# Kernel tuning notes

Hardware: AMD Instinct MI355X
Metric: run time of the kernel (lower is better)

Reference implementation:

```python
import math
import jax, jax.numpy as jnp
import numpy as np

INPUT_DIM = 1024
OUTPUT_DIM = 1024
DEGREE = 8
EPS = 1.0


def setup_inputs() -> dict:
    key = jax.random.key(0)
    k1, k2 = jax.random.split(key)
    x = jax.random.normal(k1, (8192, INPUT_DIM), dtype=jnp.float32)
    std = 1.0 / (INPUT_DIM * (DEGREE + 1))
    hermite_coeffs = std * jax.random.normal(k2, (INPUT_DIM, OUTPUT_DIM, DEGREE + 1), dtype=jnp.float32)
    return {"x": x, "hermite_coeffs": hermite_coeffs}


def _hermite_basis(x):
    # x: [B, I] squashed input; returns [B, I, DEGREE+1] Hermite-function basis.
    pi_q = math.pi ** (-0.25)
    gauss = jnp.exp(-0.5 * x * x)
    h0 = pi_q * gauss
    hs = [h0]
    if DEGREE > 0:
        hs.append(math.sqrt(2.0) * pi_q * x * gauss)
    for i in range(2, DEGREE + 1):
        hs.append(math.sqrt(2.0 / i) * x * hs[i - 1] - math.sqrt((i - 1) / i) * hs[i - 2])
    return jnp.stack(hs, axis=-1)


def reference(x, hermite_coeffs):
    x = x.reshape(-1, INPUT_DIM)
    x = jnp.tanh(x) * (math.sqrt(2 * DEGREE + 1) + EPS)
    hermite = _hermite_basis(x)  # [B, I, D+1]
    y = jnp.einsum('bid,iod->bo', hermite, hermite_coeffs)
    return y.reshape(-1, OUTPUT_DIM)
```

## Files before the change

### kernel.cpp

```cpp
#include <hip/hip_runtime.h>

#define MDIM 8192
#define IDIM 1024
#define ODIM 1024
#define D1   9
#define KDIM (IDIM * D1)

typedef _Float16 half8 __attribute__((ext_vector_type(8)));
typedef float    float4v __attribute__((ext_vector_type(4)));

#define BSCALE 256.0f
#define INV_BSCALE (1.0f / 256.0f)

__device__ __forceinline__ void hermite9(float xv, float h[D1]) {
    float ax = fabsf(xv);
    float t  = __expf(-2.0f * ax);
    float th = (1.0f - t) / (1.0f + t);
    th = copysignf(th, xv);
    float u = th * 5.123105625617661f;
    float g = __expf(-0.5f * u * u);
    h[0] = 0.7511255444649425f * g;
    h[1] = 1.0622519497598084f * u * g;
    const float c1[D1] = {0.f, 0.f, 1.0f, 0.8164965809277260f, 0.7071067811865476f,
                          0.6324555320336759f, 0.5773502691896258f, 0.5345224838248488f, 0.5f};
    const float c2[D1] = {0.f, 0.f, 0.7071067811865476f, 0.8164965809277260f, 0.8660254037844386f,
                          0.8944271909999159f, 0.9128709291752769f, 0.9258200997725514f, 0.9354143466934853f};
#pragma unroll
    for (int d = 2; d < D1; ++d) h[d] = c1[d] * u * h[d - 1] - c2[d] * h[d - 2];
}

__global__ void prep_b(const float* __restrict__ C, _Float16* __restrict__ Bt) {
    int t = blockIdx.x * 256 + threadIdx.x;
    int o = t >> 10;
    int i = t & 1023;
    const float* cp = C + ((size_t)i * ODIM + o) * D1;
    _Float16* bp = Bt + (size_t)o * KDIM + i;
#pragma unroll
    for (int d = 0; d < D1; ++d)
        bp[(size_t)d * IDIM] = (_Float16)(cp[d] * BSCALE);
}

__global__ void prep_h(const float* __restrict__ x, _Float16* __restrict__ H,
                       int row0, int nrows) {
    int t = blockIdx.x * 256 + threadIdx.x;
    int r = t >> 7;
    int ig = (t & 127) << 3;
    if (r >= nrows) return;
    const float* xp = x + ((size_t)(row0 + r) << 10) + ig;
    float4 a0 = *(const float4*)xp;
    float4 a1 = *(const float4*)(xp + 4);
    float xv[8] = {a0.x, a0.y, a0.z, a0.w, a1.x, a1.y, a1.z, a1.w};
    float h[8][D1];
#pragma unroll
    for (int e = 0; e < 8; ++e) hermite9(xv[e], h[e]);
    _Float16* hp = H + (size_t)r * KDIM + ig;
#pragma unroll
    for (int d = 0; d < D1; ++d) {
        half8 v;
#pragma unroll
        for (int e = 0; e < 8; ++e) v[e] = (_Float16)h[e][d];
        *(half8*)(hp + (size_t)d * IDIM) = v;
    }
}

__global__ __launch_bounds__(256, 2) void gemm_hf(
    const _Float16* __restrict__ A,
    const _Float16* __restrict__ Bt,
    float* __restrict__ out)
{
    const int tid = threadIdx.x;
    const int w = tid >> 6;
    const int l = tid & 63;
    const int bn = blockIdx.x;
    const int bm = blockIdx.y;

    __shared__ _Float16 As[128 * 64];
    __shared__ _Float16 Bs[128 * 64];

    const int lrow8 = l >> 3;
    const int kgrp  = (l & 7) ^ lrow8;
    const _Float16* Ag = A  + ((size_t)(bm * 128 + w * 8 + lrow8) * KDIM + kgrp * 8);
    const _Float16* Bg = Bt + ((size_t)(bn * 128 + w * 8 + lrow8) * KDIM + kgrp * 8);

    const int q   = l >> 4;
    const int m16 = l & 15;
    const int s3  = m16 & 7;
    const int wm  = w >> 1, wn = w & 1;

    float4v acc[4][4] = {};

    for (int k0 = 0; k0 < KDIM; k0 += 64) {
#pragma unroll
        for (int r = 0; r < 4; ++r) {
            __builtin_amdgcn_global_load_lds(
                (const __attribute__((address_space(1))) void*)(Ag + (size_t)(r * 32) * KDIM + k0),
                (__attribute__((address_space(3))) void*)((char*)As + (r * 4 + w) * 1024),
                16, 0, 0);
            __builtin_amdgcn_global_load_lds(
                (const __attribute__((address_space(1))) void*)(Bg + (size_t)(r * 32) * KDIM + k0),
                (__attribute__((address_space(3))) void*)((char*)Bs + (r * 4 + w) * 1024),
                16, 0, 0);
        }
        __syncthreads();

#pragma unroll
        for (int ko = 0; ko < 2; ++ko) {
            const int slot = (q + 4 * ko) ^ s3;
            half8 af[4], bf[4];
#pragma unroll
            for (int i = 0; i < 4; ++i) {
                af[i] = *(const half8*)&As[(wm * 64 + i * 16 + m16) * 64 + slot * 8];
                bf[i] = *(const half8*)&Bs[(wn * 64 + i * 16 + m16) * 64 + slot * 8];
            }
#pragma unroll
            for (int i = 0; i < 4; ++i)
#pragma unroll
                for (int j = 0; j < 4; ++j)
                    acc[i][j] = __builtin_amdgcn_mfma_f32_16x16x32_f16(af[i], bf[j], acc[i][j], 0, 0, 0);
        }
        __syncthreads();
    }

#pragma unroll
    for (int i = 0; i < 4; ++i) {
        int row = bm * 128 + wm * 64 + i * 16 + q * 4;
#pragma unroll
        for (int j = 0; j < 4; ++j) {
            int col = bn * 128 + wn * 64 + j * 16 + m16;
            float* op = out + (size_t)row * ODIM + col;
#pragma unroll
            for (int r2 = 0; r2 < 4; ++r2)
                op[(size_t)r2 * ODIM] = acc[i][j][r2] * INV_BSCALE;
        }
    }
}

__global__ void naive_kernel(const float* __restrict__ x, const float* __restrict__ C,
                             float* __restrict__ out) {
    __shared__ float hb[IDIM * D1];
    int b = blockIdx.x;
    int tid = threadIdx.x;
    for (int i = tid; i < IDIM; i += 256) {
        float h[D1];
        hermite9(x[(size_t)b * IDIM + i], h);
#pragma unroll
        for (int d = 0; d < D1; ++d) hb[i * D1 + d] = h[d];
    }
    __syncthreads();
    for (int o = tid; o < ODIM; o += 256) {
        float acc = 0.f;
        for (int i = 0; i < IDIM; ++i) {
            const float* cp = C + ((size_t)i * ODIM + o) * D1;
            const float* hp = hb + i * D1;
#pragma unroll
            for (int d = 0; d < D1; ++d) acc += hp[d] * cp[d];
        }
        out[(size_t)b * ODIM + o] = acc;
    }
}

extern "C" void kernel_launch(void* const* d_in, const int* in_sizes, int n_in,
                              void* d_out, int out_size, void* d_ws, size_t ws_size,
                              hipStream_t stream) {
    const float* x      = (const float*)d_in[0];
    const float* coeffs = (const float*)d_in[1];
    float* out = (float*)d_out;

    const size_t bt_bytes = (size_t)ODIM * KDIM * sizeof(_Float16);
    size_t avail = ws_size > bt_bytes ? ws_size - bt_bytes : 0;
    long rows = (long)(avail / ((size_t)KDIM * sizeof(_Float16)));
    rows = (rows / 128) * 128;
    if (rows > MDIM) rows = MDIM;

    if (rows >= 128) {
        _Float16* Bt = (_Float16*)d_ws;
        _Float16* H  = (_Float16*)((char*)d_ws + bt_bytes);
        hipLaunchKernelGGL(prep_b, dim3((IDIM * ODIM) / 256), dim3(256), 0, stream, coeffs, Bt);
        for (int row0 = 0; row0 < MDIM; row0 += (int)rows) {
            int nr = (MDIM - row0) < rows ? (MDIM - row0) : (int)rows;
            hipLaunchKernelGGL(prep_h, dim3(nr / 2), dim3(256), 0, stream, x, H, row0, nr);
            hipLaunchKernelGGL(gemm_hf, dim3(8, nr / 128), dim3(256), 0, stream,
                               H, Bt, out + (size_t)row0 * ODIM);
        }
    } else {
        hipLaunchKernelGGL(naive_kernel, dim3(MDIM), dim3(256), 0, stream, x, coeffs, out);
    }
}
```

Baseline: 306.5 us.

## Fuse Hermite basis generation into GEMM and tile coefficient transpose via LDS

Removes the materialized fp16 Hermite matrix H (8192x9216) and computes the basis inside the GEMM kernel. Each block loads x once per 64-input chunk, evaluates tanh/gauss in fp32, and runs the degree recurrence in packed fp16 while streaming B slices per degree. prep_b is rewritten to transpose through shared memory so global accesses coalesce. The cost is recomputing the basis in each of the 8 column blocks, extra VALU work and barriers inside the GEMM loop, and lower precision in the fp16 recurrence.

```diff
diff --git a/kernel.cpp b/kernel.cpp
--- a/kernel.cpp
+++ b/kernel.cpp
@@ -6,21 +6,25 @@
 #define D1   9
 #define KDIM (IDIM * D1)
 
-typedef _Float16 half8 __attribute__((ext_vector_type(8)));
+typedef _Float16 half8   __attribute__((ext_vector_type(8)));
+typedef _Float16 half2v  __attribute__((ext_vector_type(2)));
 typedef float    float4v __attribute__((ext_vector_type(4)));
 
 #define BSCALE 256.0f
 #define INV_BSCALE (1.0f / 256.0f)
+#define USCALE 5.123105625617661f
+#define H0C 0.7511255444649425f
+#define H1C 1.0622519497598084f
 
 __device__ __forceinline__ void hermite9(float xv, float h[D1]) {
     float ax = fabsf(xv);
     float t  = __expf(-2.0f * ax);
     float th = (1.0f - t) / (1.0f + t);
     th = copysignf(th, xv);
-    float u = th * 5.123105625617661f;
+    float u = th * USCALE;
     float g = __expf(-0.5f * u * u);
-    h[0] = 0.7511255444649425f * g;
-    h[1] = 1.0622519497598084f * u * g;
+    h[0] = H0C * g;
+    h[1] = H1C * u * g;
     const float c1[D1] = {0.f, 0.f, 1.0f, 0.8164965809277260f, 0.7071067811865476f,
                           0.6324555320336759f, 0.5773502691896258f, 0.5345224838248488f, 0.5f};
     const float c2[D1] = {0.f, 0.f, 0.7071067811865476f, 0.8164965809277260f, 0.8660254037844386f,
@@ -29,42 +33,35 @@
     for (int d = 2; d < D1; ++d) h[d] = c1[d] * u * h[d - 1] - c2[d] * h[d - 2];
 }
 
-__global__ void prep_b(const float* __restrict__ C, _Float16* __restrict__ Bt) {
-    int t = blockIdx.x * 256 + threadIdx.x;
-    int o = t >> 10;
-    int i = t & 1023;
-    const float* cp = C + ((size_t)i * ODIM + o) * D1;
-    _Float16* bp = Bt + (size_t)o * KDIM + i;
-#pragma unroll
-    for (int d = 0; d < D1; ++d)
-        bp[(size_t)d * IDIM] = (_Float16)(cp[d] * BSCALE);
-}
-
-__global__ void prep_h(const float* __restrict__ x, _Float16* __restrict__ H,
-                       int row0, int nrows) {
-    int t = blockIdx.x * 256 + threadIdx.x;
-    int r = t >> 7;
-    int ig = (t & 127) << 3;
-    if (r >= nrows) return;
-    const float* xp = x + ((size_t)(row0 + r) << 10) + ig;
-    float4 a0 = *(const float4*)xp;
-    float4 a1 = *(const float4*)(xp + 4);
-    float xv[8] = {a0.x, a0.y, a0.z, a0.w, a1.x, a1.y, a1.z, a1.w};
-    float h[8][D1];
-#pragma unroll
-    for (int e = 0; e < 8; ++e) hermite9(xv[e], h[e]);
-    _Float16* hp = H + (size_t)r * KDIM + ig;
-#pragma unroll
-    for (int d = 0; d < D1; ++d) {
-        half8 v;
-#pragma unroll
-        for (int e = 0; e < 8; ++e) v[e] = (_Float16)h[e][d];
-        *(half8*)(hp + (size_t)d * IDIM) = v;
-    }
-}
-
-__global__ __launch_bounds__(256, 2) void gemm_hf(
-    const _Float16* __restrict__ A,
+__global__ __launch_bounds__(256) void prep_b(const float* __restrict__ C,
+                                              _Float16* __restrict__ Bt) {
+    __shared__ float lds[288 * 33];
+    const int t  = threadIdx.x;
+    const int ti = blockIdx.x & 31;
+    const int to = blockIdx.x >> 5;
+    const float* base = C + (size_t)ti * 32 * 9216 + (size_t)to * 32 * 9;
+#pragma unroll
+    for (int j = 0; j < 36; ++j) {
+        int f   = t + 256 * j;
+        int row = f / 288;
+        int col = f - row * 288;
+        lds[col * 33 + row] = base[(size_t)row * 9216 + col];
+    }
+    __syncthreads();
+    _Float16* bb = Bt + (size_t)to * 32 * KDIM + ti * 32;
+#pragma unroll
+    for (int j = 0; j < 36; ++j) {
+        int e   = t + 256 * j;
+        int i   = e & 31;
+        int odp = e >> 5;
+        int ol  = odp / 9;
+        int d   = odp - ol * 9;
+        bb[(size_t)ol * KDIM + d * IDIM + i] = (_Float16)(lds[odp * 33 + i] * BSCALE);
+    }
+}
+
+__global__ __launch_bounds__(256, 2) void gemm_fused(
+    const float* __restrict__ x,
     const _Float16* __restrict__ Bt,
     float* __restrict__ out)
 {
@@ -79,7 +76,6 @@
 
     const int lrow8 = l >> 3;
     const int kgrp  = (l & 7) ^ lrow8;
-    const _Float16* Ag = A  + ((size_t)(bm * 128 + w * 8 + lrow8) * KDIM + kgrp * 8);
     const _Float16* Bg = Bt + ((size_t)(bn * 128 + w * 8 + lrow8) * KDIM + kgrp * 8);
 
     const int q   = l >> 4;
@@ -87,38 +83,111 @@
     const int s3  = m16 & 7;
     const int wm  = w >> 1, wn = w & 1;
 
+    const int r  = tid >> 1;
+    const int ih = tid & 1;
+    const int r7 = r & 7;
+    _Float16* arow = As + r * 64;
+
     float4v acc[4][4] = {};
 
-    for (int k0 = 0; k0 < KDIM; k0 += 64) {
-#pragma unroll
-        for (int r = 0; r < 4; ++r) {
+    constexpr float c1a[D1] = {0.f, 0.f, 1.0f, 0.8164965809277260f, 0.7071067811865476f,
+                               0.6324555320336759f, 0.5773502691896258f, 0.5345224838248488f, 0.5f};
+    constexpr float c2a[D1] = {0.f, 0.f, 0.7071067811865476f, 0.8164965809277260f, 0.8660254037844386f,
+                               0.8944271909999159f, 0.9128709291752769f, 0.9258200997725514f, 0.9354143466934853f};
+
+    for (int ib = 0; ib < 16; ++ib) {
+        const int kbase = ib * 64;
+
+#pragma unroll
+        for (int rr = 0; rr < 4; ++rr)
             __builtin_amdgcn_global_load_lds(
-                (const __attribute__((address_space(1))) void*)(Ag + (size_t)(r * 32) * KDIM + k0),
-                (__attribute__((address_space(3))) void*)((char*)As + (r * 4 + w) * 1024),
+                (const __attribute__((address_space(1))) void*)(Bg + (size_t)(rr * 32) * KDIM + kbase),
+                (__attribute__((address_space(3))) void*)((char*)Bs + (rr * 4 + w) * 1024),
                 16, 0, 0);
-            __builtin_amdgcn_global_load_lds(
-                (const __attribute__((address_space(1))) void*)(Bg + (size_t)(r * 32) * KDIM + k0),
-                (__attribute__((address_space(3))) void*)((char*)Bs + (r * 4 + w) * 1024),
-                16, 0, 0);
-        }
-        __syncthreads();
-
-#pragma unroll
-        for (int ko = 0; ko < 2; ++ko) {
-            const int slot = (q + 4 * ko) ^ s3;
-            half8 af[4], bf[4];
-#pragma unroll
-            for (int i = 0; i < 4; ++i) {
-                af[i] = *(const half8*)&As[(wm * 64 + i * 16 + m16) * 64 + slot * 8];
-                bf[i] = *(const half8*)&Bs[(wn * 64 + i * 16 + m16) * 64 + slot * 8];
-            }
-#pragma unroll
-            for (int i = 0; i < 4; ++i)
-#pragma unroll
-                for (int j = 0; j < 4; ++j)
-                    acc[i][j] = __builtin_amdgcn_mfma_f32_16x16x32_f16(af[i], bf[j], acc[i][j], 0, 0, 0);
-        }
-        __syncthreads();
+
+        const float4* xp = (const float4*)(x + (((size_t)(bm * 128 + r)) << 10) + kbase + ih * 32);
+        float u[32];
+#pragma unroll
+        for (int j = 0; j < 8; ++j) {
+            float4 v = xp[j];
+            u[4*j+0] = v.x; u[4*j+1] = v.y; u[4*j+2] = v.z; u[4*j+3] = v.w;
+        }
+#pragma unroll
+        for (int j = 0; j < 32; ++j) {
+            float xv = u[j];
+            float t2 = __expf(-2.0f * fabsf(xv));
+            float th = (1.0f - t2) / (1.0f + t2);
+            u[j] = copysignf(th, xv) * USCALE;
+        }
+        half2v u2[16], hA[16], hB[16];
+#pragma unroll
+        for (int p = 0; p < 16; ++p) {
+            float u0 = u[2*p], u1 = u[2*p+1];
+            float g0 = __expf(-0.5f * u0 * u0);
+            float g1 = __expf(-0.5f * u1 * u1);
+            u2[p] = half2v{(_Float16)u0, (_Float16)u1};
+            hA[p] = half2v{(_Float16)(H0C * g0), (_Float16)(H0C * g1)};
+            hB[p] = half2v{(_Float16)(H1C * u0 * g0), (_Float16)(H1C * u1 * g1)};
+        }
+
+#pragma unroll
+        for (int d = 0; d < D1; ++d) {
+            if (d >= 1) {
+#pragma unroll
+                for (int rr = 0; rr < 4; ++rr)
+                    __builtin_amdgcn_global_load_lds(
+                        (const __attribute__((address_space(1))) void*)(Bg + (size_t)(rr * 32) * KDIM + d * IDIM + kbase),
+                        (__attribute__((address_space(3))) void*)((char*)Bs + (rr * 4 + w) * 1024),
+                        16, 0, 0);
+            }
+            half2v ht[16];
+            if (d == 0) {
+#pragma unroll
+                for (int p = 0; p < 16; ++p) ht[p] = hA[p];
+            } else if (d == 1) {
+#pragma unroll
+                for (int p = 0; p < 16; ++p) ht[p] = hB[p];
+            } else {
+                const half2v c1v = half2v{(_Float16)c1a[d], (_Float16)c1a[d]};
+                const half2v c2v = half2v{(_Float16)c2a[d], (_Float16)c2a[d]};
+#pragma unroll
+                for (int p = 0; p < 16; ++p) {
+                    half2v t = u2[p] * hB[p];
+                    ht[p] = c1v * t - c2v * hA[p];
+                    hA[p] = hB[p];
+                    hB[p] = ht[p];
+                }
+            }
+#pragma unroll
+            for (int c = 0; c < 4; ++c) {
+                int slot = (ih * 4 + c) ^ r7;
+                half8 vv;
+#pragma unroll
+                for (int pp = 0; pp < 4; ++pp) {
+                    vv[2*pp+0] = ht[4*c+pp][0];
+                    vv[2*pp+1] = ht[4*c+pp][1];
+                }
+                *(half8*)(arow + slot * 8) = vv;
+            }
+            __syncthreads();
+
+#pragma unroll
+            for (int ko = 0; ko < 2; ++ko) {
+                const int slot = (q + 4 * ko) ^ s3;
+                half8 af[4], bf[4];
+#pragma unroll
+                for (int i = 0; i < 4; ++i) {
+                    af[i] = *(const half8*)&As[(wm * 64 + i * 16 + m16) * 64 + slot * 8];
+                    bf[i] = *(const half8*)&Bs[(wn * 64 + i * 16 + m16) * 64 + slot * 8];
+                }
+#pragma unroll
+                for (int i = 0; i < 4; ++i)
+#pragma unroll
+                    for (int j = 0; j < 4; ++j)
+                        acc[i][j] = __builtin_amdgcn_mfma_f32_16x16x32_f16(af[i], bf[j], acc[i][j], 0, 0, 0);
+            }
+            __syncthreads();
+        }
     }
 
 #pragma unroll
@@ -167,21 +236,11 @@
     float* out = (float*)d_out;
 
     const size_t bt_bytes = (size_t)ODIM * KDIM * sizeof(_Float16);
-    size_t avail = ws_size > bt_bytes ? ws_size - bt_bytes : 0;
-    long rows = (long)(avail / ((size_t)KDIM * sizeof(_Float16)));
-    rows = (rows / 128) * 128;
-    if (rows > MDIM) rows = MDIM;
-
-    if (rows >= 128) {
+
+    if (ws_size >= bt_bytes) {
         _Float16* Bt = (_Float16*)d_ws;
-        _Float16* H  = (_Float16*)((char*)d_ws + bt_bytes);
-        hipLaunchKernelGGL(prep_b, dim3((IDIM * ODIM) / 256), dim3(256), 0, stream, coeffs, Bt);
-        for (int row0 = 0; row0 < MDIM; row0 += (int)rows) {
-            int nr = (MDIM - row0) < rows ? (MDIM - row0) : (int)rows;
-            hipLaunchKernelGGL(prep_h, dim3(nr / 2), dim3(256), 0, stream, x, H, row0, nr);
-            hipLaunchKernelGGL(gemm_hf, dim3(8, nr / 128), dim3(256), 0, stream,
-                               H, Bt, out + (size_t)row0 * ODIM);
-        }
+        hipLaunchKernelGGL(prep_b, dim3(1024), dim3(256), 0, stream, coeffs, Bt);
+        hipLaunchKernelGGL(gemm_fused, dim3(8, 64), dim3(256), 0, stream, x, Bt, out);
     } else {
         hipLaunchKernelGGL(naive_kernel, dim3(MDIM), dim3(256), 0, stream, x, coeffs, out);
     }
```

After: 313.9 us. 2.4% more time.

## Split-K GEMM with atomics, fuse prep kernels, transpose coeffs via LDS

Applied to the files above, without the earlier changes.

Merges the coefficient-repack and Hermite-basis preparation into one launch. The coefficient repack now goes through a padded LDS tile so that global reads and writes are coalesced. The GEMM is split along K into two halves via a z grid dimension, and partial results are combined with float atomicAdd into an output that is zeroed first by a memset. Launch bounds rise to 4 blocks per CU for more occupancy. These aim to fill more CUs with 1024 blocks and to cut prep overhead, at the cost of atomic traffic, an extra memset, and nondeterministic summation order.

```diff
diff --git a/kernel.cpp b/kernel.cpp
--- a/kernel.cpp
+++ b/kernel.cpp
@@ -5,65 +5,86 @@
 #define ODIM 1024
 #define D1   9
 #define KDIM (IDIM * D1)
-
-typedef _Float16 half8 __attribute__((ext_vector_type(8)));
+#define KHALF (KDIM / 2)
+
+typedef _Float16 half8   __attribute__((ext_vector_type(8)));
 typedef float    float4v __attribute__((ext_vector_type(4)));
 
 #define BSCALE 256.0f
 #define INV_BSCALE (1.0f / 256.0f)
+#define USCALE 5.123105625617661f
+#define H0C 0.7511255444649425f
+#define SQRT2 1.4142135623730951f
+
+__constant__ float c1a[D1] = {0.f, 0.f, 1.0f, 0.8164965809277260f, 0.7071067811865476f,
+                              0.6324555320336759f, 0.5773502691896258f, 0.5345224838248488f, 0.5f};
+__constant__ float c2a[D1] = {0.f, 0.f, 0.7071067811865476f, 0.8164965809277260f, 0.8660254037844386f,
+                              0.8944271909999159f, 0.9128709291752769f, 0.9258200997725514f, 0.9354143466934853f};
 
 __device__ __forceinline__ void hermite9(float xv, float h[D1]) {
     float ax = fabsf(xv);
     float t  = __expf(-2.0f * ax);
-    float th = (1.0f - t) / (1.0f + t);
+    float th = (1.0f - t) * __builtin_amdgcn_rcpf(1.0f + t);
     th = copysignf(th, xv);
-    float u = th * 5.123105625617661f;
+    float u = th * USCALE;
     float g = __expf(-0.5f * u * u);
-    h[0] = 0.7511255444649425f * g;
-    h[1] = 1.0622519497598084f * u * g;
-    const float c1[D1] = {0.f, 0.f, 1.0f, 0.8164965809277260f, 0.7071067811865476f,
-                          0.6324555320336759f, 0.5773502691896258f, 0.5345224838248488f, 0.5f};
-    const float c2[D1] = {0.f, 0.f, 0.7071067811865476f, 0.8164965809277260f, 0.8660254037844386f,
-                          0.8944271909999159f, 0.9128709291752769f, 0.9258200997725514f, 0.9354143466934853f};
-#pragma unroll
-    for (int d = 2; d < D1; ++d) h[d] = c1[d] * u * h[d - 1] - c2[d] * h[d - 2];
-}
-
-__global__ void prep_b(const float* __restrict__ C, _Float16* __restrict__ Bt) {
-    int t = blockIdx.x * 256 + threadIdx.x;
-    int o = t >> 10;
-    int i = t & 1023;
-    const float* cp = C + ((size_t)i * ODIM + o) * D1;
-    _Float16* bp = Bt + (size_t)o * KDIM + i;
-#pragma unroll
-    for (int d = 0; d < D1; ++d)
-        bp[(size_t)d * IDIM] = (_Float16)(cp[d] * BSCALE);
-}
-
-__global__ void prep_h(const float* __restrict__ x, _Float16* __restrict__ H,
-                       int row0, int nrows) {
-    int t = blockIdx.x * 256 + threadIdx.x;
-    int r = t >> 7;
-    int ig = (t & 127) << 3;
-    if (r >= nrows) return;
-    const float* xp = x + ((size_t)(row0 + r) << 10) + ig;
-    float4 a0 = *(const float4*)xp;
-    float4 a1 = *(const float4*)(xp + 4);
-    float xv[8] = {a0.x, a0.y, a0.z, a0.w, a1.x, a1.y, a1.z, a1.w};
-    float h[8][D1];
-#pragma unroll
-    for (int e = 0; e < 8; ++e) hermite9(xv[e], h[e]);
-    _Float16* hp = H + (size_t)r * KDIM + ig;
-#pragma unroll
-    for (int d = 0; d < D1; ++d) {
-        half8 v;
-#pragma unroll
-        for (int e = 0; e < 8; ++e) v[e] = (_Float16)h[e][d];
-        *(half8*)(hp + (size_t)d * IDIM) = v;
-    }
-}
-
-__global__ __launch_bounds__(256, 2) void gemm_hf(
+    h[0] = H0C * g;
+    h[1] = SQRT2 * H0C * u * g;
+#pragma unroll
+    for (int d = 2; d < D1; ++d) h[d] = c1a[d] * u * h[d - 1] - c2a[d] * h[d - 2];
+}
+
+__global__ __launch_bounds__(256) void prep_all(const float* __restrict__ C,
+                                                _Float16* __restrict__ Bt,
+                                                const float* __restrict__ x,
+                                                _Float16* __restrict__ H) {
+    if (blockIdx.x < 1024) {
+        __shared__ float lds[288 * 33];
+        const int t  = threadIdx.x;
+        const int ti = blockIdx.x & 31;
+        const int to = blockIdx.x >> 5;
+        const float* base = C + (size_t)ti * 32 * 9216 + (size_t)to * 32 * 9;
+#pragma unroll
+        for (int j = 0; j < 36; ++j) {
+            int f   = t + 256 * j;
+            int row = f / 288;
+            int col = f - row * 288;
+            lds[col * 33 + row] = base[(size_t)row * 9216 + col];
+        }
+        __syncthreads();
+        _Float16* bb = Bt + (size_t)to * 32 * KDIM + ti * 32;
+#pragma unroll
+        for (int j = 0; j < 36; ++j) {
+            int e   = t + 256 * j;
+            int i   = e & 31;
+            int odp = e >> 5;
+            int ol  = odp / 9;
+            int d   = odp - ol * 9;
+            bb[(size_t)ol * KDIM + d * IDIM + i] = (_Float16)(lds[odp * 33 + i] * BSCALE);
+        }
+    } else {
+        int t  = (blockIdx.x - 1024) * 256 + threadIdx.x;
+        int r  = t >> 7;
+        int ig = (t & 127) << 3;
+        const float* xp = x + (((size_t)r) << 10) + ig;
+        float4 a0 = *(const float4*)xp;
+        float4 a1 = *(const float4*)(xp + 4);
+        float xv[8] = {a0.x, a0.y, a0.z, a0.w, a1.x, a1.y, a1.z, a1.w};
+        float h[8][D1];
+#pragma unroll
+        for (int e = 0; e < 8; ++e) hermite9(xv[e], h[e]);
+        _Float16* hp = H + (size_t)r * KDIM + ig;
+#pragma unroll
+        for (int d = 0; d < D1; ++d) {
+            half8 v;
+#pragma unroll
+            for (int e = 0; e < 8; ++e) v[e] = (_Float16)h[e][d];
+            *(half8*)(hp + (size_t)d * IDIM) = v;
+        }
+    }
+}
+
+__global__ __launch_bounds__(256, 4) void gemm_hf(
     const _Float16* __restrict__ A,
     const _Float16* __restrict__ Bt,
     float* __restrict__ out)
@@ -73,14 +94,15 @@
     const int l = tid & 63;
     const int bn = blockIdx.x;
     const int bm = blockIdx.y;
+    const int kb0 = blockIdx.z * KHALF;
 
     __shared__ _Float16 As[128 * 64];
     __shared__ _Float16 Bs[128 * 64];
 
     const int lrow8 = l >> 3;
     const int kgrp  = (l & 7) ^ lrow8;
-    const _Float16* Ag = A  + ((size_t)(bm * 128 + w * 8 + lrow8) * KDIM + kgrp * 8);
-    const _Float16* Bg = Bt + ((size_t)(bn * 128 + w * 8 + lrow8) * KDIM + kgrp * 8);
+    const _Float16* Ag = A  + ((size_t)(bm * 128 + w * 8 + lrow8) * KDIM + kb0 + kgrp * 8);
+    const _Float16* Bg = Bt + ((size_t)(bn * 128 + w * 8 + lrow8) * KDIM + kb0 + kgrp * 8);
 
     const int q   = l >> 4;
     const int m16 = l & 15;
@@ -89,7 +111,7 @@
 
     float4v acc[4][4] = {};
 
-    for (int k0 = 0; k0 < KDIM; k0 += 64) {
+    for (int k0 = 0; k0 < KHALF; k0 += 64) {
 #pragma unroll
         for (int r = 0; r < 4; ++r) {
             __builtin_amdgcn_global_load_lds(
@@ -130,7 +152,7 @@
             float* op = out + (size_t)row * ODIM + col;
 #pragma unroll
             for (int r2 = 0; r2 < 4; ++r2)
-                op[(size_t)r2 * ODIM] = acc[i][j][r2] * INV_BSCALE;
+                atomicAdd(op + (size_t)r2 * ODIM, acc[i][j][r2] * INV_BSCALE);
         }
     }
 }
@@ -167,21 +189,15 @@
     float* out = (float*)d_out;
 
     const size_t bt_bytes = (size_t)ODIM * KDIM * sizeof(_Float16);
-    size_t avail = ws_size > bt_bytes ? ws_size - bt_bytes : 0;
-    long rows = (long)(avail / ((size_t)KDIM * sizeof(_Float16)));
-    rows = (rows / 128) * 128;
-    if (rows > MDIM) rows = MDIM;
-
-    if (rows >= 128) {
+    const size_t h_bytes  = (size_t)MDIM * KDIM * sizeof(_Float16);
+
+    if (ws_size >= bt_bytes + h_bytes) {
         _Float16* Bt = (_Float16*)d_ws;
         _Float16* H  = (_Float16*)((char*)d_ws + bt_bytes);
-        hipLaunchKernelGGL(prep_b, dim3((IDIM * ODIM) / 256), dim3(256), 0, stream, coeffs, Bt);
-        for (int row0 = 0; row0 < MDIM; row0 += (int)rows) {
-            int nr = (MDIM - row0) < rows ? (MDIM - row0) : (int)rows;
-            hipLaunchKernelGGL(prep_h, dim3(nr / 2), dim3(256), 0, stream, x, H, row0, nr);
-            hipLaunchKernelGGL(gemm_hf, dim3(8, nr / 128), dim3(256), 0, stream,
-                               H, Bt, out + (size_t)row0 * ODIM);
-        }
+        hipMemsetAsync(out, 0, (size_t)out_size * sizeof(float), stream);
+        hipLaunchKernelGGL(prep_all, dim3(1024 + (MDIM * IDIM) / 2048), dim3(256), 0, stream,
+                           coeffs, Bt, x, H);
+        hipLaunchKernelGGL(gemm_hf, dim3(8, 64, 2), dim3(256), 0, stream, H, Bt, out);
     } else {
         hipLaunchKernelGGL(naive_kernel, dim3(MDIM), dim3(256), 0, stream, x, coeffs, out);
     }
```

Result: slower. 331.4 us (+8.1%).
